# Kernel tuning notes

Measured on AMD Instinct MI355X. Metric: run time of the kernel, lower is better.

The kernel has to match this reference:

```python
import jax, jax.numpy as jnp
import numpy as np

N = 6144          # num utterances (graph nodes)
D = 128           # utt_embed_size
WIN = 10          # att_window_size
NUM_SPK = 8
N_EMO = 7


def _init(key, shape):
    fan_in = shape[0]
    return jax.random.normal(key, shape, dtype=jnp.float32) * (1.0 / np.sqrt(fan_in))


def setup_inputs() -> dict:
    key = jax.random.key(0)
    ks = jax.random.split(key, 20)
    inp = {
        "x": jax.random.normal(ks[0], (N, D), dtype=jnp.float32),
        "speakers": jax.random.randint(ks[1], (N,), 0, NUM_SPK, dtype=jnp.int32),
        # layer-1 relation GCN weights (pred / suc / same / diff)
        "W_pred1": _init(ks[2], (D, D)),
        "W_suc1": _init(ks[3], (D, D)),
        "W_same1": _init(ks[4], (D, D)),
        "W_diff1": _init(ks[5], (D, D)),
        # layer-2 relation GCN weights
        "W_pred2": _init(ks[6], (D, D)),
        "W_suc2": _init(ks[7], (D, D)),
        "W_same2": _init(ks[8], (D, D)),
        "W_diff2": _init(ks[9], (D, D)),
        "w_aggr_1": _init(ks[10], (D, D)),
        "w_aggr_2": _init(ks[11], (D, D)),
        "w_e1": _init(ks[12], (2 * D, D)),
        "b_e1": jnp.zeros((D,), dtype=jnp.float32),
        "w_e2": _init(ks[13], (D, N_EMO)),
        "b_e2": jnp.zeros((N_EMO,), dtype=jnp.float32),
        "w_s": _init(ks[14], (2 * D, N_EMO)),
        "b_s": jnp.zeros((N_EMO,), dtype=jnp.float32),
    }
    return inp


def reference(x, speakers, W_pred1, W_suc1, W_same1, W_diff1,
              W_pred2, W_suc2, W_same2, W_diff2,
              w_aggr_1, w_aggr_2, w_e1, b_e1, w_e2, b_e2, w_s, b_s):
    n = x.shape[0]
    idx = jnp.arange(n)
    # windowed dot-product attention; entries outside the window stay 0.0
    # BEFORE the softmax (faithful to the torch code: zeros, not -inf)
    band = jnp.abs(idx[:, None] - idx[None, :]) <= WIN
    scores = jnp.where(band, x @ x.T, 0.0)            # [N, N]
    attn = jax.nn.softmax(scores, axis=1)
    # relation masks
    same = (speakers[:, None] == speakers[None, :]).astype(x.dtype)
    pred = (idx[None, :] >= idx[:, None]).astype(x.dtype)   # triu incl diag
    suc = 1.0 - pred                                          # strict lower tri
    adjs = (same * pred * attn,        # same-speaker, predecessor
            same * suc * attn,         # same-speaker, successor
            (1.0 - same) * pred * attn,  # diff-speaker, predecessor
            (1.0 - same) * suc * attn)   # diff-speaker, successor

    def gcn(h, Ws):  # sum_k adj_k @ (h @ W_k)
        return sum(a @ (h @ w) for a, w in zip(adjs, Ws))

    d = jnp.diagonal(attn)[:, None]   # self-attention scale
    h1 = jax.nn.relu(gcn(x, (W_pred1, W_suc1, W_same1, W_diff1))
                     + (x @ w_aggr_1) * d)
    h2 = jax.nn.relu(gcn(h1, (W_pred2, W_suc2, W_same2, W_diff2))
                     + (h1 @ w_aggr_2) * d)
    h = jnp.concatenate([h2, x], axis=1)              # [N, 2D]
    emotion = jax.nn.relu(h @ w_e1 + b_e1) @ w_e2 + b_e2   # [N, 7]
    sentiment = h @ w_s + b_s                               # [N, 7]
    return emotion, sentiment
```

## Files before the change

kernel.cpp:

```cpp
#include <hip/hip_runtime.h>
#include <hip/hip_bf16.h>


#define NN   6144
#define DD   128
#define WINW 10
#define YST  168
#define TAB_OFF 27456
#define SS_OFF  33088
#define SM_BYTES 35904
#define NBLK 768
#define WS_W1T 0
#define WS_W2T 163840
#define WS_WE1 327680
#define WS_WE2 393216
#define WS_WST 397312
#define WS_H1  405504
#define WS_H2  1978368
#define BAR_OFF 3551232
#define F1_OFF 16384
#define F2_OFF 40960
#define BAR_BYTES 65536

typedef unsigned short u16;
typedef unsigned long long u64;
typedef __attribute__((ext_vector_type(8))) short bf16x8;
typedef __attribute__((ext_vector_type(4))) float f32x4;

__device__ __forceinline__ float b2f(u16 u) {
    return __uint_as_float(((unsigned int)u) << 16);
}
__device__ __forceinline__ u16 f2b(float f) {
    __hip_bfloat16 h = __float2bfloat16(f);
    return *reinterpret_cast<u16*>(&h);
}
__device__ __forceinline__ bf16x8 cvt8(const float* p) {
    float4 u = *reinterpret_cast<const float4*>(p);
    float4 v = *reinterpret_cast<const float4*>(p + 4);
    bf16x8 r;
    r[0] = (short)f2b(u.x); r[1] = (short)f2b(u.y);
    r[2] = (short)f2b(u.z); r[3] = (short)f2b(u.w);
    r[4] = (short)f2b(v.x); r[5] = (short)f2b(v.y);
    r[6] = (short)f2b(v.z); r[7] = (short)f2b(v.w);
    return r;
}
__device__ __forceinline__ void st_agent_u32(unsigned* p, unsigned v) {
    __hip_atomic_store(p, v, __ATOMIC_RELAXED, __HIP_MEMORY_SCOPE_AGENT);
}
__device__ __forceinline__ void st_agent_u64(u64* p, u64 v) {
    __hip_atomic_store(p, v, __ATOMIC_RELAXED, __HIP_MEMORY_SCOPE_AGENT);
}
__device__ __forceinline__ unsigned ld_agent_u32(const unsigned* p) {
    return __hip_atomic_load(p, __ATOMIC_RELAXED, __HIP_MEMORY_SCOPE_AGENT);
}
__device__ __forceinline__ unsigned add_agent_u32(unsigned* p, unsigned v) {
    return __hip_atomic_fetch_add(p, v, __ATOMIC_RELAXED,
                                  __HIP_MEMORY_SCOPE_AGENT);
}
__device__ __forceinline__ void poll_ge(unsigned* p, unsigned v) {
    while (ld_agent_u32(p) < v) __builtin_amdgcn_s_sleep(1);
}
__device__ __forceinline__ const float* sel5(int r,
    const float* a0, const float* a1, const float* a2,
    const float* a3, const float* a4) {
    return r == 0 ? a0 : r == 1 ? a1 : r == 2 ? a2 : r == 3 ? a3 : a4;
}

__device__ __forceinline__ void layer_tile(
    const float* __restrict__ x, const u16* __restrict__ Ab16,
    const u16* __restrict__ BT, const int* __restrict__ spk,
    u16* __restrict__ hout, int first_layer, int hb, int bm,
    char* smraw, int tid, char* gate, int bid)
{
    u16*   Ys  = (u16*)smraw;
    float* Xs  = (float*)smraw;
    int2*  tab = (int2*)(smraw + TAB_OFF);
    float* Ss  = (float*)(smraw + SS_OFF);
    const int wave = tid >> 6, lane = tid & 63;
    const int lm = lane & 15, quad = lane >> 4;
    const int wm = wave >> 1, wn = wave & 1;

    bf16x8 afr[2][4];

    if (first_layer) {
        #pragma unroll
        for (int it = 0; it < 7; ++it) {
            int f = tid + it * 256;
            if (f < 52 * 32) {
                int s = f >> 5, c = f & 31;
                int g = min(max(bm - WINW + s, 0), NN - 1);
                *reinterpret_cast<float4*>(&Xs[s * 132 + c * 4]) =
                    *reinterpret_cast<const float4*>(&x[(size_t)g * DD + c * 4]);
            }
        }
        __syncthreads();

        if (tid < 128) {
            const int il = tid >> 2, q = tid & 3;
            const float* xr = &Xs[(il + WINW) * 132 + q * 32];
            float4 xq[8];
            #pragma unroll
            for (int c = 0; c < 8; ++c)
                xq[c] = *reinterpret_cast<const float4*>(xr + c * 4);
            float po[21];
            #pragma unroll
            for (int o = 0; o < 21; ++o) {
                const float* jr = &Xs[(il + o) * 132 + q * 32];
                float a0 = 0.f, a1 = 0.f, a2 = 0.f, a3 = 0.f;
                #pragma unroll
                for (int c = 0; c < 8; ++c) {
                    float4 b = *reinterpret_cast<const float4*>(jr + c * 4);
                    a0 = fmaf(xq[c].x, b.x, a0); a1 = fmaf(xq[c].y, b.y, a1);
                    a2 = fmaf(xq[c].z, b.z, a2); a3 = fmaf(xq[c].w, b.w, a3);
                }
                po[o] = (a0 + a1) + (a2 + a3);
            }
            #pragma unroll
            for (int o = 0; o < 21; ++o) {
                po[o] += __shfl_xor(po[o], 1);
                po[o] += __shfl_xor(po[o], 2);
            }
            if (q == 0) {
                #pragma unroll
                for (int o = 0; o < 21; ++o) {
                    int jg = bm + il - WINW + o;
                    Ss[il * 22 + o] =
                        (jg >= 0 && jg < NN) ? po[o] : -1e30f;
                }
            }
        }
        __syncthreads();

        if (tid < 32) {
            int il = tid, i = bm + il;
            float m = 0.f;
            #pragma unroll
            for (int o = 0; o < 21; ++o) {
                float s = Ss[il * 22 + o];
                if (s > -1e29f) m = fmaxf(m, s);
            }
            int lo = i - WINW; if (lo < 0) lo = 0;
            int hi = i + WINW; if (hi > NN - 1) hi = NN - 1;
            float Z = (float)(NN - (hi - lo + 1)) * __expf(-m);
            float ev[21];
            #pragma unroll
            for (int o = 0; o < 21; ++o) {
                float s = Ss[il * 22 + o];
                ev[o] = (s > -1e29f) ? __expf(s - m) : 0.f;
                Z += ev[o];
            }
            float rz = 1.f / Z;
            #pragma unroll
            for (int o = 0; o < 21; ++o) Ss[il * 22 + o] = ev[o] * rz;
        }
        __syncthreads();

        #pragma unroll
        for (int rr = 0; rr < 3; ++rr) {
            int p = tid + rr * 256;
            if (p < 704) {
                int il = p / 22, e = p - il * 22;
                int i  = bm + il;
                int si = spk[i];
                float w; int off;
                if (e < 21) {
                    int j = i - WINW + e;
                    bool valid = (j >= 0) && (j < NN);
                    int jc  = valid ? j : i;
                    int sel = (spk[jc] == si) ? ((j >= i) ? 0 : 1)
                                              : ((j >= i) ? 2 : 3);
                    w   = valid ? Ss[il * 22 + e] : 0.f;
                    off = valid ? (il + e) * YST + sel * 32 : 0;
                } else {
                    w   = Ss[il * 22 + WINW];
                    off = (il + WINW) * YST + 4 * 32;
                }
                tab[p] = make_int2(__float_as_int(w), off);
            }
        }

        #pragma unroll
        for (int mt = 0; mt < 2; ++mt) {
            int rl = min((wm * 2 + mt) * 16 + lm, 51);
            #pragma unroll
            for (int s = 0; s < 4; ++s)
                afr[mt][s] = cvt8(&Xs[rl * 132 + s * 32 + quad * 8]);
        }
        __syncthreads();

        if (gate) {
            if (tid == 0) {
                unsigned g = (unsigned)bid >> 5;
                unsigned* gflag = (unsigned*)(gate + 8192 + g * 128);
                unsigned* rflag = (unsigned*)(gate + 12288);
                if ((bid & 31) == 0) {
                    poll_ge(rflag, 1u);
                    st_agent_u32(gflag, 1u);
                } else {
                    poll_ge(gflag, 1u);
                }
            }
            __syncthreads();
            __builtin_amdgcn_sched_barrier(0);
        }
    } else {
        #pragma unroll
        for (int mt = 0; mt < 2; ++mt) {
            int gr = min(max(bm - WINW + (wm * 2 + mt) * 16 + lm, 0), NN - 1);
            #pragma unroll
            for (int s = 0; s < 4; ++s)
                afr[mt][s] = *reinterpret_cast<const bf16x8*>(
                    Ab16 + (size_t)gr * DD + s * 32 + quad * 8);
        }
    }

    f32x4 acc[2][5];
    #pragma unroll
    for (int mt = 0; mt < 2; ++mt)
        #pragma unroll
        for (int n = 0; n < 5; ++n) acc[mt][n] = {0.f, 0.f, 0.f, 0.f};

    #pragma unroll
    for (int np = 0; np < 5; ++np) {
        int nt = wn * 5 + np;
        int gn = (nt >> 1) * 128 + hb * 32 + (nt & 1) * 16 + lm;
        #pragma unroll
        for (int s = 0; s < 4; ++s) {
            bf16x8 b = *reinterpret_cast<const bf16x8*>(
                BT + (size_t)gn * DD + s * 32 + quad * 8);
            acc[0][np] = __builtin_amdgcn_mfma_f32_16x16x32_bf16(afr[0][s], b, acc[0][np], 0, 0, 0);
            acc[1][np] = __builtin_amdgcn_mfma_f32_16x16x32_bf16(afr[1][s], b, acc[1][np], 0, 0, 0);
        }
    }
    #pragma unroll
    for (int mt = 0; mt < 2; ++mt)
        #pragma unroll
        for (int np = 0; np < 5; ++np) {
            int nt = wn * 5 + np;
            #pragma unroll
            for (int r = 0; r < 4; ++r) {
                int lr = (wm * 2 + mt) * 16 + quad * 4 + r;
                if (lr < 52) Ys[lr * YST + nt * 16 + lm] = f2b(acc[mt][np][r]);
            }
        }
    __syncthreads();

    {
        const int c0 = (tid & 7) * 4;
        const int il = tid >> 3;
        float a0 = 0.f, a1 = 0.f, a2 = 0.f, a3 = 0.f;
        const int2* tp = &tab[il * 22];
        #pragma unroll
        for (int e = 0; e < 22; ++e) {
            int2 t = tp[e];
            float w = __int_as_float(t.x);
            u64 y4 = *reinterpret_cast<const u64*>(Ys + t.y + c0);
            a0 = fmaf(w, b2f((u16)(y4 & 0xffff)), a0);
            a1 = fmaf(w, b2f((u16)((y4 >> 16) & 0xffff)), a1);
            a2 = fmaf(w, b2f((u16)((y4 >> 32) & 0xffff)), a2);
            a3 = fmaf(w, b2f((u16)(y4 >> 48)), a3);
        }
        int i = bm + il;
        u64 pk = (u64)f2b(fmaxf(a0, 0.f)) |
                 ((u64)f2b(fmaxf(a1, 0.f)) << 16) |
                 ((u64)f2b(fmaxf(a2, 0.f)) << 32) |
                 ((u64)f2b(fmaxf(a3, 0.f)) << 48);
        st_agent_u64(reinterpret_cast<u64*>(
            &hout[(size_t)i * DD + hb * 32 + c0]), pk);
    }
}

__global__ __launch_bounds__(256, 4) void fused_kernel(
    const float* __restrict__ x, const int* __restrict__ spk,
    const float* __restrict__ p0, const float* __restrict__ p1,
    const float* __restrict__ p2, const float* __restrict__ p3,
    const float* __restrict__ p4,
    const float* __restrict__ q0, const float* __restrict__ q1,
    const float* __restrict__ q2, const float* __restrict__ q3,
    const float* __restrict__ q4,
    const float* __restrict__ we1, const float* __restrict__ be1,
    const float* __restrict__ we2, const float* __restrict__ be2,
    const float* __restrict__ wss, const float* __restrict__ bss,
    float* __restrict__ out, char* __restrict__ ws)
{
    u16*   W1T   = (u16*)(ws + WS_W1T);
    u16*   W2T   = (u16*)(ws + WS_W2T);
    u16*   We1T  = (u16*)(ws + WS_WE1);
    u16*   we2T  = (u16*)(ws + WS_WE2);
    u16*   wsT   = (u16*)(ws + WS_WST);
    u16*   h1b   = (u16*)(ws + WS_H1);
    u16*   h2b   = (u16*)(ws + WS_H2);
    char*  bar   = ws + BAR_OFF;
    unsigned* flag1 = (unsigned*)(bar + F1_OFF);
    unsigned* flag2 = (unsigned*)(bar + F2_OFF);

    __shared__ __align__(16) char smraw[SM_BYTES];
    const int bid = blockIdx.x;
    const int tid = threadIdx.x;

    if (bid < 160) {
        unsigned* W1T32 = (unsigned*)W1T;
        unsigned* W2T32 = (unsigned*)W2T;
        int idx = bid * 256 + tid;
        int c = idx & 127, rk = idx >> 7;
        int r = rk >> 6, k2 = rk & 63, k = k2 * 2;
        const float* s1 = sel5(r, p0, p1, p2, p3, p4);
        const float* s2 = sel5(r, q0, q1, q2, q3, q4);
        unsigned v1 = (unsigned)f2b(s1[k * 128 + c]) |
                      ((unsigned)f2b(s1[(k + 1) * 128 + c]) << 16);
        unsigned v2 = (unsigned)f2b(s2[k * 128 + c]) |
                      ((unsigned)f2b(s2[(k + 1) * 128 + c]) << 16);
        int U = (r * 128 + c) * 64 + k2;
        st_agent_u32(&W1T32[U], v1);
        st_agent_u32(&W2T32[U], v2);
    } else if (bid < 192) {
        unsigned* We1T32 = (unsigned*)We1T;
        #pragma unroll
        for (int it = 0; it < 2; ++it) {
            int idx = (bid - 160) * 256 + tid + it * 8192;
            int n = idx & 127, k2 = idx >> 7, k = k2 * 2;
            unsigned v = (unsigned)f2b(we1[k * 128 + n]) |
                         ((unsigned)f2b(we1[(k + 1) * 128 + n]) << 16);
            st_agent_u32(&We1T32[n * 128 + k2], v);
        }
    } else if (bid == 192) {
        unsigned* we2T32 = (unsigned*)we2T;
        #pragma unroll
        for (int it = 0; it < 4; ++it) {
            int U = tid + it * 256;
            int n = U >> 6, kh = U & 63, k = kh * 2;
            float lo = n < 7 ? we2[k * 7 + n] : 0.f;
            float hi = n < 7 ? we2[(k + 1) * 7 + n] : 0.f;
            st_agent_u32(&we2T32[U],
                         (unsigned)f2b(lo) | ((unsigned)f2b(hi) << 16));
        }
    } else if (bid == 193) {
        unsigned* wsT32 = (unsigned*)wsT;
        #pragma unroll
        for (int it = 0; it < 8; ++it) {
            int U = tid + it * 256;
            int n = U >> 7, kh = U & 127, k = kh * 2;
            float lo = n < 7 ? wss[k * 7 + n] : 0.f;
            float hi = n < 7 ? wss[(k + 1) * 7 + n] : 0.f;
            st_agent_u32(&wsT32[U],
                         (unsigned)f2b(lo) | ((unsigned)f2b(hi) << 16));
        }
    }

    __syncthreads();
    if (tid == 0) {
        unsigned g = (unsigned)bid >> 5;
        unsigned* gctr = (unsigned*)(bar + g * 128);
        unsigned* rctr = (unsigned*)(bar + 4096);
        unsigned* rflag = (unsigned*)(bar + 12288);
        unsigned r = add_agent_u32(gctr, 1u);
        if (r == 31u) {
            unsigned rr = add_agent_u32(rctr, 1u);
            if (rr == 23u) st_agent_u32(rflag, 1u);
        }
    }

    const int hb = bid / 192, bmi = bid - hb * 192;
    const int bm = bmi * 32;
    layer_tile(x, nullptr, W1T, spk, h1b, 1, hb, bm, smraw, tid, bar, bid);

    __syncthreads();
    if (tid == 0) add_agent_u32(&flag1[bmi * 32], 1u);
    if (tid == 0) {
        if (bmi > 0)   poll_ge(&flag1[(bmi - 1) * 32], 4u);
        poll_ge(&flag1[bmi * 32], 4u);
        if (bmi < 191) poll_ge(&flag1[(bmi + 1) * 32], 4u);
    }
    __syncthreads();
    __builtin_amdgcn_sched_barrier(0);

    layer_tile(nullptr, h1b, W2T, spk, h2b, 0, hb, bm, smraw, tid, nullptr, bid);

    __syncthreads();
    if (tid == 0) add_agent_u32(&flag2[bmi * 32], 1u);

    if (bid < 384) {
        const int rt = (bid & ~15) | ((bid & 7) << 1) | ((bid >> 3) & 1);
        const int bmh = rt * 16;
        const int wave = tid >> 6, lane = tid & 63;
        const int lm = lane & 15, quad = lane >> 4;
        const int row = bmh + lm;

        bf16x8 afr[8];
        #pragma unroll
        for (int s = 4; s < 8; ++s)
            afr[s] = cvt8(&x[(size_t)row * DD + (s - 4) * 32 + quad * 8]);
        if (tid == 0) poll_ge(&flag2[(rt >> 1) * 32], 4u);
        __syncthreads();
        __builtin_amdgcn_sched_barrier(0);

        #pragma unroll
        for (int s = 0; s < 4; ++s)
            afr[s] = *reinterpret_cast<const bf16x8*>(
                &h2b[(size_t)row * DD + s * 32 + quad * 8]);

        float* Es = (float*)smraw;
        f32x4 accE[2], accS = {0.f, 0.f, 0.f, 0.f};
        #pragma unroll
        for (int n = 0; n < 2; ++n) accE[n] = {0.f, 0.f, 0.f, 0.f};

        #pragma unroll
        for (int s = 0; s < 8; ++s) {
            #pragma unroll
            for (int n = 0; n < 2; ++n) {
                int nt = wave * 2 + n;
                bf16x8 b = *reinterpret_cast<const bf16x8*>(
                    &We1T[(size_t)(nt * 16 + lm) * 256 + s * 32 + quad * 8]);
                accE[n] = __builtin_amdgcn_mfma_f32_16x16x32_bf16(afr[s], b, accE[n], 0, 0, 0);
            }
            if (wave == 0) {
                bf16x8 bsf = *reinterpret_cast<const bf16x8*>(
                    &wsT[(size_t)lm * 256 + s * 32 + quad * 8]);
                accS = __builtin_amdgcn_mfma_f32_16x16x32_bf16(afr[s], bsf, accS, 0, 0, 0);
            }
        }

        if (wave == 0 && lm < 7) {
            #pragma unroll
            for (int r = 0; r < 4; ++r) {
                int i = bmh + quad * 4 + r;
                out[(size_t)NN * 7 + (size_t)i * 7 + lm] = accS[r] + bss[lm];
            }
        }
        #pragma unroll
        for (int n = 0; n < 2; ++n) {
            int col = (wave * 2 + n) * 16 + lm;
            float bias = be1[col];
            #pragma unroll
            for (int r = 0; r < 4; ++r)
                Es[(quad * 4 + r) * 132 + col] = fmaxf(accE[n][r] + bias, 0.f);
        }
        __syncthreads();

        if (wave == 0) {
            f32x4 accM = {0.f, 0.f, 0.f, 0.f};
            #pragma unroll
            for (int s = 0; s < 4; ++s) {
                bf16x8 a = cvt8(&Es[lm * 132 + s * 32 + quad * 8]);
                bf16x8 b = *reinterpret_cast<const bf16x8*>(
                    &we2T[(size_t)lm * 128 + s * 32 + quad * 8]);
                accM = __builtin_amdgcn_mfma_f32_16x16x32_bf16(a, b, accM, 0, 0, 0);
            }
            if (lm < 7) {
                #pragma unroll
                for (int r = 0; r < 4; ++r) {
                    int i = bmh + quad * 4 + r;
                    out[(size_t)i * 7 + lm] = accM[r] + be2[lm];
                }
            }
        }
    }
}

extern "C" void kernel_launch(void* const* d_in, const int* in_sizes, int n_in,
                              void* d_out, int out_size, void* d_ws, size_t ws_size,
                              hipStream_t stream)
{
    const float* x   = (const float*)d_in[0];
    const int*   spk = (const int*)d_in[1];
    const float* Wp1 = (const float*)d_in[2];
    const float* Wu1 = (const float*)d_in[3];
    const float* Wm1 = (const float*)d_in[4];
    const float* Wd1 = (const float*)d_in[5];
    const float* Wp2 = (const float*)d_in[6];
    const float* Wu2 = (const float*)d_in[7];
    const float* Wm2 = (const float*)d_in[8];
    const float* Wd2 = (const float*)d_in[9];
    const float* wa1 = (const float*)d_in[10];
    const float* wa2 = (const float*)d_in[11];
    const float* we1 = (const float*)d_in[12];
    const float* be1 = (const float*)d_in[13];
    const float* we2 = (const float*)d_in[14];
    const float* be2 = (const float*)d_in[15];
    const float* wss = (const float*)d_in[16];
    const float* bss = (const float*)d_in[17];
    float* out = (float*)d_out;
    char*  ws  = (char*)d_ws;

    hipMemsetAsync(ws + BAR_OFF, 0, BAR_BYTES, stream);

    fused_kernel<<<dim3(NBLK), dim3(256), 0, stream>>>(
        x, spk, Wp1, Wu1, Wm1, Wd1, wa1, Wp2, Wu2, Wm2, Wd2, wa2,
        we1, be1, we2, be2, wss, bss, out, ws);
}
```

Measured before the change: 146.4 us.

## Recompute halo rows per block to remove inter-block layer barriers

Each block now owns 8 output rows and recomputes attention, layer-1 activations over a 28-row halo, and layer 2 entirely in LDS. This removes the global h1/h2 buffers and the cross-block flag polling between layers. Adjacency tables are regrouped by relation so each 128-column weight slice is applied in turn. The cost is redundant halo computation (about 3.5x the layer-1 rows) and lower occupancy from launch bounds 4 to 3 with more LDS.

```diff
diff --git a/kernel.cpp b/kernel.cpp
--- a/kernel.cpp
+++ b/kernel.cpp
@@ -5,22 +5,31 @@
 #define NN   6144
 #define DD   128
 #define WINW 10
-#define YST  168
-#define TAB_OFF 27456
-#define SS_OFF  33088
-#define SM_BYTES 35904
+#define OROWS 8
+#define SROWS 48
+#define HROWS 28
+#define XST  132
+#define YST2 132
+#define H1ST 136
 #define NBLK 768
+#define NPACK 194
+#define LDS_A    0
+#define LDS_SS   25344
+#define LDS_TAB1 27808
+#define LDS_ST1  32736
+#define LDS_TAB2 33408
+#define LDS_ST2  34816
+#define LDS_H1   35008
+#define LDS_H2   42624
+#define LDS_SPK  44800
+#define SM_BYTES 44992
 #define WS_W1T 0
 #define WS_W2T 163840
 #define WS_WE1 327680
 #define WS_WE2 393216
 #define WS_WST 397312
-#define WS_H1  405504
-#define WS_H2  1978368
 #define BAR_OFF 3551232
-#define F1_OFF 16384
-#define F2_OFF 40960
-#define BAR_BYTES 65536
+#define BAR_BYTES 16384
 
 typedef unsigned short u16;
 typedef unsigned long long u64;
@@ -47,9 +56,6 @@
 __device__ __forceinline__ void st_agent_u32(unsigned* p, unsigned v) {
     __hip_atomic_store(p, v, __ATOMIC_RELAXED, __HIP_MEMORY_SCOPE_AGENT);
 }
-__device__ __forceinline__ void st_agent_u64(u64* p, u64 v) {
-    __hip_atomic_store(p, v, __ATOMIC_RELAXED, __HIP_MEMORY_SCOPE_AGENT);
-}
 __device__ __forceinline__ unsigned ld_agent_u32(const unsigned* p) {
     return __hip_atomic_load(p, __ATOMIC_RELAXED, __HIP_MEMORY_SCOPE_AGENT);
 }
@@ -65,212 +71,18 @@
     const float* a3, const float* a4) {
     return r == 0 ? a0 : r == 1 ? a1 : r == 2 ? a2 : r == 3 ? a3 : a4;
 }
-
-__device__ __forceinline__ void layer_tile(
-    const float* __restrict__ x, const u16* __restrict__ Ab16,
-    const u16* __restrict__ BT, const int* __restrict__ spk,
-    u16* __restrict__ hout, int first_layer, int hb, int bm,
-    char* smraw, int tid, char* gate, int bid)
-{
-    u16*   Ys  = (u16*)smraw;
-    float* Xs  = (float*)smraw;
-    int2*  tab = (int2*)(smraw + TAB_OFF);
-    float* Ss  = (float*)(smraw + SS_OFF);
-    const int wave = tid >> 6, lane = tid & 63;
-    const int lm = lane & 15, quad = lane >> 4;
-    const int wm = wave >> 1, wn = wave & 1;
-
-    bf16x8 afr[2][4];
-
-    if (first_layer) {
-        #pragma unroll
-        for (int it = 0; it < 7; ++it) {
-            int f = tid + it * 256;
-            if (f < 52 * 32) {
-                int s = f >> 5, c = f & 31;
-                int g = min(max(bm - WINW + s, 0), NN - 1);
-                *reinterpret_cast<float4*>(&Xs[s * 132 + c * 4]) =
-                    *reinterpret_cast<const float4*>(&x[(size_t)g * DD + c * 4]);
-            }
-        }
-        __syncthreads();
-
-        if (tid < 128) {
-            const int il = tid >> 2, q = tid & 3;
-            const float* xr = &Xs[(il + WINW) * 132 + q * 32];
-            float4 xq[8];
-            #pragma unroll
-            for (int c = 0; c < 8; ++c)
-                xq[c] = *reinterpret_cast<const float4*>(xr + c * 4);
-            float po[21];
-            #pragma unroll
-            for (int o = 0; o < 21; ++o) {
-                const float* jr = &Xs[(il + o) * 132 + q * 32];
-                float a0 = 0.f, a1 = 0.f, a2 = 0.f, a3 = 0.f;
-                #pragma unroll
-                for (int c = 0; c < 8; ++c) {
-                    float4 b = *reinterpret_cast<const float4*>(jr + c * 4);
-                    a0 = fmaf(xq[c].x, b.x, a0); a1 = fmaf(xq[c].y, b.y, a1);
-                    a2 = fmaf(xq[c].z, b.z, a2); a3 = fmaf(xq[c].w, b.w, a3);
-                }
-                po[o] = (a0 + a1) + (a2 + a3);
-            }
-            #pragma unroll
-            for (int o = 0; o < 21; ++o) {
-                po[o] += __shfl_xor(po[o], 1);
-                po[o] += __shfl_xor(po[o], 2);
-            }
-            if (q == 0) {
-                #pragma unroll
-                for (int o = 0; o < 21; ++o) {
-                    int jg = bm + il - WINW + o;
-                    Ss[il * 22 + o] =
-                        (jg >= 0 && jg < NN) ? po[o] : -1e30f;
-                }
-            }
-        }
-        __syncthreads();
-
-        if (tid < 32) {
-            int il = tid, i = bm + il;
-            float m = 0.f;
-            #pragma unroll
-            for (int o = 0; o < 21; ++o) {
-                float s = Ss[il * 22 + o];
-                if (s > -1e29f) m = fmaxf(m, s);
-            }
-            int lo = i - WINW; if (lo < 0) lo = 0;
-            int hi = i + WINW; if (hi > NN - 1) hi = NN - 1;
-            float Z = (float)(NN - (hi - lo + 1)) * __expf(-m);
-            float ev[21];
-            #pragma unroll
-            for (int o = 0; o < 21; ++o) {
-                float s = Ss[il * 22 + o];
-                ev[o] = (s > -1e29f) ? __expf(s - m) : 0.f;
-                Z += ev[o];
-            }
-            float rz = 1.f / Z;
-            #pragma unroll
-            for (int o = 0; o < 21; ++o) Ss[il * 22 + o] = ev[o] * rz;
-        }
-        __syncthreads();
-
-        #pragma unroll
-        for (int rr = 0; rr < 3; ++rr) {
-            int p = tid + rr * 256;
-            if (p < 704) {
-                int il = p / 22, e = p - il * 22;
-                int i  = bm + il;
-                int si = spk[i];
-                float w; int off;
-                if (e < 21) {
-                    int j = i - WINW + e;
-                    bool valid = (j >= 0) && (j < NN);
-                    int jc  = valid ? j : i;
-                    int sel = (spk[jc] == si) ? ((j >= i) ? 0 : 1)
-                                              : ((j >= i) ? 2 : 3);
-                    w   = valid ? Ss[il * 22 + e] : 0.f;
-                    off = valid ? (il + e) * YST + sel * 32 : 0;
-                } else {
-                    w   = Ss[il * 22 + WINW];
-                    off = (il + WINW) * YST + 4 * 32;
-                }
-                tab[p] = make_int2(__float_as_int(w), off);
-            }
-        }
-
-        #pragma unroll
-        for (int mt = 0; mt < 2; ++mt) {
-            int rl = min((wm * 2 + mt) * 16 + lm, 51);
-            #pragma unroll
-            for (int s = 0; s < 4; ++s)
-                afr[mt][s] = cvt8(&Xs[rl * 132 + s * 32 + quad * 8]);
-        }
-        __syncthreads();
-
-        if (gate) {
-            if (tid == 0) {
-                unsigned g = (unsigned)bid >> 5;
-                unsigned* gflag = (unsigned*)(gate + 8192 + g * 128);
-                unsigned* rflag = (unsigned*)(gate + 12288);
-                if ((bid & 31) == 0) {
-                    poll_ge(rflag, 1u);
-                    st_agent_u32(gflag, 1u);
-                } else {
-                    poll_ge(gflag, 1u);
-                }
-            }
-            __syncthreads();
-            __builtin_amdgcn_sched_barrier(0);
-        }
-    } else {
-        #pragma unroll
-        for (int mt = 0; mt < 2; ++mt) {
-            int gr = min(max(bm - WINW + (wm * 2 + mt) * 16 + lm, 0), NN - 1);
-            #pragma unroll
-            for (int s = 0; s < 4; ++s)
-                afr[mt][s] = *reinterpret_cast<const bf16x8*>(
-                    Ab16 + (size_t)gr * DD + s * 32 + quad * 8);
-        }
-    }
-
-    f32x4 acc[2][5];
-    #pragma unroll
-    for (int mt = 0; mt < 2; ++mt)
-        #pragma unroll
-        for (int n = 0; n < 5; ++n) acc[mt][n] = {0.f, 0.f, 0.f, 0.f};
-
-    #pragma unroll
-    for (int np = 0; np < 5; ++np) {
-        int nt = wn * 5 + np;
-        int gn = (nt >> 1) * 128 + hb * 32 + (nt & 1) * 16 + lm;
-        #pragma unroll
-        for (int s = 0; s < 4; ++s) {
-            bf16x8 b = *reinterpret_cast<const bf16x8*>(
-                BT + (size_t)gn * DD + s * 32 + quad * 8);
-            acc[0][np] = __builtin_amdgcn_mfma_f32_16x16x32_bf16(afr[0][s], b, acc[0][np], 0, 0, 0);
-            acc[1][np] = __builtin_amdgcn_mfma_f32_16x16x32_bf16(afr[1][s], b, acc[1][np], 0, 0, 0);
-        }
-    }
-    #pragma unroll
-    for (int mt = 0; mt < 2; ++mt)
-        #pragma unroll
-        for (int np = 0; np < 5; ++np) {
-            int nt = wn * 5 + np;
-            #pragma unroll
-            for (int r = 0; r < 4; ++r) {
-                int lr = (wm * 2 + mt) * 16 + quad * 4 + r;
-                if (lr < 52) Ys[lr * YST + nt * 16 + lm] = f2b(acc[mt][np][r]);
-            }
-        }
-    __syncthreads();
-
-    {
-        const int c0 = (tid & 7) * 4;
-        const int il = tid >> 3;
-        float a0 = 0.f, a1 = 0.f, a2 = 0.f, a3 = 0.f;
-        const int2* tp = &tab[il * 22];
-        #pragma unroll
-        for (int e = 0; e < 22; ++e) {
-            int2 t = tp[e];
-            float w = __int_as_float(t.x);
-            u64 y4 = *reinterpret_cast<const u64*>(Ys + t.y + c0);
-            a0 = fmaf(w, b2f((u16)(y4 & 0xffff)), a0);
-            a1 = fmaf(w, b2f((u16)((y4 >> 16) & 0xffff)), a1);
-            a2 = fmaf(w, b2f((u16)((y4 >> 32) & 0xffff)), a2);
-            a3 = fmaf(w, b2f((u16)(y4 >> 48)), a3);
-        }
-        int i = bm + il;
-        u64 pk = (u64)f2b(fmaxf(a0, 0.f)) |
-                 ((u64)f2b(fmaxf(a1, 0.f)) << 16) |
-                 ((u64)f2b(fmaxf(a2, 0.f)) << 32) |
-                 ((u64)f2b(fmaxf(a3, 0.f)) << 48);
-        st_agent_u64(reinterpret_cast<u64*>(
-            &hout[(size_t)i * DD + hb * 32 + c0]), pk);
-    }
-}
-
-__global__ __launch_bounds__(256, 4) void fused_kernel(
+__device__ __forceinline__ void acc4_add(f32x4& a, float w, u64 y4) {
+    a[0] = fmaf(w, b2f((u16)(y4 & 0xffff)), a[0]);
+    a[1] = fmaf(w, b2f((u16)((y4 >> 16) & 0xffff)), a[1]);
+    a[2] = fmaf(w, b2f((u16)((y4 >> 32) & 0xffff)), a[2]);
+    a[3] = fmaf(w, b2f((u16)(y4 >> 48)), a[3]);
+}
+__device__ __forceinline__ u64 pack4_relu(f32x4 a) {
+    return (u64)f2b(fmaxf(a[0], 0.f)) | ((u64)f2b(fmaxf(a[1], 0.f)) << 16) |
+           ((u64)f2b(fmaxf(a[2], 0.f)) << 32) | ((u64)f2b(fmaxf(a[3], 0.f)) << 48);
+}
+
+__global__ __launch_bounds__(256, 3) void fused_kernel(
     const float* __restrict__ x, const int* __restrict__ spk,
     const float* __restrict__ p0, const float* __restrict__ p1,
     const float* __restrict__ p2, const float* __restrict__ p3,
@@ -283,20 +95,30 @@
     const float* __restrict__ wss, const float* __restrict__ bss,
     float* __restrict__ out, char* __restrict__ ws)
 {
-    u16*   W1T   = (u16*)(ws + WS_W1T);
-    u16*   W2T   = (u16*)(ws + WS_W2T);
-    u16*   We1T  = (u16*)(ws + WS_WE1);
-    u16*   we2T  = (u16*)(ws + WS_WE2);
-    u16*   wsT   = (u16*)(ws + WS_WST);
-    u16*   h1b   = (u16*)(ws + WS_H1);
-    u16*   h2b   = (u16*)(ws + WS_H2);
-    char*  bar   = ws + BAR_OFF;
-    unsigned* flag1 = (unsigned*)(bar + F1_OFF);
-    unsigned* flag2 = (unsigned*)(bar + F2_OFF);
+    u16* W1T  = (u16*)(ws + WS_W1T);
+    u16* W2T  = (u16*)(ws + WS_W2T);
+    u16* We1T = (u16*)(ws + WS_WE1);
+    u16* we2T = (u16*)(ws + WS_WE2);
+    u16* wsT  = (u16*)(ws + WS_WST);
+    char* bar = ws + BAR_OFF;
 
     __shared__ __align__(16) char smraw[SM_BYTES];
-    const int bid = blockIdx.x;
-    const int tid = threadIdx.x;
+    float* Xs  = (float*)(smraw + LDS_A);
+    u16*   Ys  = (u16*)(smraw + LDS_A);
+    float* Es  = (float*)(smraw + LDS_A);
+    float* Ss  = (float*)(smraw + LDS_SS);
+    int2*  tab1 = (int2*)(smraw + LDS_TAB1);
+    int*   st1  = (int*)(smraw + LDS_ST1);
+    int2*  tab2 = (int2*)(smraw + LDS_TAB2);
+    int*   st2  = (int*)(smraw + LDS_ST2);
+    u16*   h1   = (u16*)(smraw + LDS_H1);
+    u16*   h2   = (u16*)(smraw + LDS_H2);
+    int*   SpkS = (int*)(smraw + LDS_SPK);
+
+    const int bid = blockIdx.x, tid = threadIdx.x;
+    const int wave = tid >> 6, lane = tid & 63;
+    const int lm = lane & 15, quad = lane >> 4;
+    const int bm = bid * OROWS;
 
     if (bid < 160) {
         unsigned* W1T32 = (unsigned*)W1T;
@@ -346,60 +168,302 @@
                          (unsigned)f2b(lo) | ((unsigned)f2b(hi) << 16));
         }
     }
-
-    __syncthreads();
+    if (bid < NPACK) {
+        __syncthreads();
+        if (tid == 0) {
+            unsigned r = add_agent_u32((unsigned*)bar, 1u);
+            if (r == NPACK - 1) st_agent_u32((unsigned*)(bar + 4096), 1u);
+        }
+    }
+
+    #pragma unroll
+    for (int it = 0; it < 6; ++it) {
+        int f = tid + it * 256;
+        int s = f >> 5, c = f & 31;
+        int g = min(max(bm - 20 + s, 0), NN - 1);
+        *reinterpret_cast<float4*>(&Xs[s * XST + c * 4]) =
+            *reinterpret_cast<const float4*>(&x[(size_t)g * DD + c * 4]);
+    }
+    if (tid < SROWS) SpkS[tid] = spk[min(max(bm - 20 + tid, 0), NN - 1)];
+    __syncthreads();
+
+    if (tid < HROWS * 8) {
+        const int hs = tid >> 3, q = tid & 7;
+        const int gc = min(max(bm - 10 + hs, 0), NN - 1);
+        const float* xr = &Xs[(gc - bm + 20) * XST + q * 16];
+        float4 xq[4];
+        #pragma unroll
+        for (int c = 0; c < 4; ++c)
+            xq[c] = *reinterpret_cast<const float4*>(xr + c * 4);
+        float po[21];
+        #pragma unroll
+        for (int o = 0; o < 21; ++o) {
+            int jg = gc - 10 + o;
+            bool valid = (jg >= 0) && (jg < NN);
+            int jl = valid ? (jg - bm + 20) : (gc - bm + 20);
+            const float* jr = &Xs[jl * XST + q * 16];
+            float a0 = 0.f, a1 = 0.f, a2 = 0.f, a3 = 0.f;
+            #pragma unroll
+            for (int c = 0; c < 4; ++c) {
+                float4 b = *reinterpret_cast<const float4*>(jr + c * 4);
+                a0 = fmaf(xq[c].x, b.x, a0); a1 = fmaf(xq[c].y, b.y, a1);
+                a2 = fmaf(xq[c].z, b.z, a2); a3 = fmaf(xq[c].w, b.w, a3);
+            }
+            po[o] = (a0 + a1) + (a2 + a3);
+        }
+        #pragma unroll
+        for (int o = 0; o < 21; ++o) {
+            po[o] += __shfl_xor(po[o], 1);
+            po[o] += __shfl_xor(po[o], 2);
+            po[o] += __shfl_xor(po[o], 4);
+        }
+        if (q == 0) {
+            #pragma unroll
+            for (int o = 0; o < 21; ++o) {
+                int jg = gc - 10 + o;
+                Ss[hs * 22 + o] = (jg >= 0 && jg < NN) ? po[o] : -1e30f;
+            }
+        }
+    }
+    __syncthreads();
+
+    if (tid < HROWS) {
+        int hs = tid, i = min(max(bm - 10 + hs, 0), NN - 1);
+        float m = 0.f;
+        #pragma unroll
+        for (int o = 0; o < 21; ++o) {
+            float s = Ss[hs * 22 + o];
+            if (s > -1e29f) m = fmaxf(m, s);
+        }
+        int lo = i - WINW; if (lo < 0) lo = 0;
+        int hi = i + WINW; if (hi > NN - 1) hi = NN - 1;
+        float Z = (float)(NN - (hi - lo + 1)) * __expf(-m);
+        float ev[21];
+        #pragma unroll
+        for (int o = 0; o < 21; ++o) {
+            float s = Ss[hs * 22 + o];
+            ev[o] = (s > -1e29f) ? __expf(s - m) : 0.f;
+            Z += ev[o];
+        }
+        float rz = 1.f / Z;
+        #pragma unroll
+        for (int o = 0; o < 21; ++o) Ss[hs * 22 + o] = ev[o] * rz;
+    }
+    __syncthreads();
+
+    if (tid < HROWS) {
+        int hs = tid;
+        int gc = min(max(bm - 10 + hs, 0), NN - 1);
+        int si = SpkS[gc - bm + 20];
+        int idx = 0;
+        for (int p = 0; p < 5; ++p) {
+            st1[hs * 6 + p] = idx;
+            for (int e = 0; e < 22; ++e) {
+                int sel; float w; int off;
+                if (e < 21) {
+                    int j = gc - 10 + e;
+                    bool valid = (j >= 0) && (j < NN);
+                    int sj = valid ? SpkS[j - bm + 20] : si;
+                    sel = (sj == si) ? ((j >= gc) ? 0 : 1)
+                                     : ((j >= gc) ? 2 : 3);
+                    w   = valid ? Ss[hs * 22 + e] : 0.f;
+                    off = valid ? (j - bm + 20) * YST2 : 0;
+                } else {
+                    sel = 4; w = Ss[hs * 22 + 10];
+                    off = (gc - bm + 20) * YST2;
+                }
+                if (sel == p) {
+                    tab1[hs * 22 + idx] = make_int2(__float_as_int(w), off);
+                    ++idx;
+                }
+            }
+        }
+        st1[hs * 6 + 5] = idx;
+    } else if (tid >= 32 && tid < 32 + OROWS) {
+        int r = tid - 32;
+        int i = bm + r;
+        int si = SpkS[r + 30];
+        si = SpkS[r + 20];
+        int idx = 0;
+        for (int p = 0; p < 5; ++p) {
+            st2[r * 6 + p] = idx;
+            for (int e = 0; e < 22; ++e) {
+                int sel; float w; int off;
+                if (e < 21) {
+                    int j = i - 10 + e;
+                    bool valid = (j >= 0) && (j < NN);
+                    int sj = valid ? SpkS[j - bm + 20] : si;
+                    sel = (sj == si) ? ((j >= i) ? 0 : 1)
+                                     : ((j >= i) ? 2 : 3);
+                    w   = valid ? Ss[(r + 10) * 22 + e] : 0.f;
+                    off = valid ? (j - bm + 10) * YST2 : 0;
+                } else {
+                    sel = 4; w = Ss[(r + 10) * 22 + 10];
+                    off = (r + 10) * YST2;
+                }
+                if (sel == p) {
+                    tab2[r * 22 + idx] = make_int2(__float_as_int(w), off);
+                    ++idx;
+                }
+            }
+        }
+        st2[r * 6 + 5] = idx;
+    }
+
+    bf16x8 afr1[3][4];
+    #pragma unroll
+    for (int mt = 0; mt < 3; ++mt) {
+        int rl = mt * 16 + lm;
+        #pragma unroll
+        for (int ks = 0; ks < 4; ++ks)
+            afr1[mt][ks] = cvt8(&Xs[rl * XST + ks * 32 + quad * 8]);
+    }
+    __syncthreads();
+
     if (tid == 0) {
         unsigned g = (unsigned)bid >> 5;
-        unsigned* gctr = (unsigned*)(bar + g * 128);
-        unsigned* rctr = (unsigned*)(bar + 4096);
-        unsigned* rflag = (unsigned*)(bar + 12288);
-        unsigned r = add_agent_u32(gctr, 1u);
-        if (r == 31u) {
-            unsigned rr = add_agent_u32(rctr, 1u);
-            if (rr == 23u) st_agent_u32(rflag, 1u);
-        }
-    }
-
-    const int hb = bid / 192, bmi = bid - hb * 192;
-    const int bm = bmi * 32;
-    layer_tile(x, nullptr, W1T, spk, h1b, 1, hb, bm, smraw, tid, bar, bid);
-
-    __syncthreads();
-    if (tid == 0) add_agent_u32(&flag1[bmi * 32], 1u);
-    if (tid == 0) {
-        if (bmi > 0)   poll_ge(&flag1[(bmi - 1) * 32], 4u);
-        poll_ge(&flag1[bmi * 32], 4u);
-        if (bmi < 191) poll_ge(&flag1[(bmi + 1) * 32], 4u);
+        unsigned* gflag = (unsigned*)(bar + 8192 + g * 128);
+        unsigned* rflag = (unsigned*)(bar + 4096);
+        if ((bid & 31) == 0) {
+            poll_ge(rflag, 1u);
+            st_agent_u32(gflag, 1u);
+        } else {
+            poll_ge(gflag, 1u);
+        }
     }
     __syncthreads();
     __builtin_amdgcn_sched_barrier(0);
 
-    layer_tile(nullptr, h1b, W2T, spk, h2b, 0, hb, bm, smraw, tid, nullptr, bid);
-
-    __syncthreads();
-    if (tid == 0) add_agent_u32(&flag2[bmi * 32], 1u);
-
-    if (bid < 384) {
-        const int rt = (bid & ~15) | ((bid & 7) << 1) | ((bid >> 3) & 1);
-        const int bmh = rt * 16;
-        const int wave = tid >> 6, lane = tid & 63;
-        const int lm = lane & 15, quad = lane >> 4;
-        const int row = bmh + lm;
-
+    f32x4 hacc[4];
+    #pragma unroll
+    for (int k = 0; k < 4; ++k) hacc[k] = {0.f, 0.f, 0.f, 0.f};
+
+    for (int p = 0; p < 5; ++p) {
+        f32x4 accY[3][2];
+        #pragma unroll
+        for (int mt = 0; mt < 3; ++mt)
+            #pragma unroll
+            for (int j = 0; j < 2; ++j) accY[mt][j] = {0.f, 0.f, 0.f, 0.f};
+        #pragma unroll
+        for (int j = 0; j < 2; ++j) {
+            int gn = p * 128 + (wave * 2 + j) * 16 + lm;
+            #pragma unroll
+            for (int ks = 0; ks < 4; ++ks) {
+                bf16x8 b = *reinterpret_cast<const bf16x8*>(
+                    W1T + (size_t)gn * 128 + ks * 32 + quad * 8);
+                #pragma unroll
+                for (int mt = 0; mt < 3; ++mt)
+                    accY[mt][j] = __builtin_amdgcn_mfma_f32_16x16x32_bf16(
+                        afr1[mt][ks], b, accY[mt][j], 0, 0, 0);
+            }
+        }
+        #pragma unroll
+        for (int mt = 0; mt < 3; ++mt)
+            #pragma unroll
+            for (int j = 0; j < 2; ++j)
+                #pragma unroll
+                for (int r = 0; r < 4; ++r) {
+                    int lr = mt * 16 + quad * 4 + r;
+                    Ys[lr * YST2 + (wave * 2 + j) * 16 + lm] =
+                        f2b(accY[mt][j][r]);
+                }
+        __syncthreads();
+        #pragma unroll
+        for (int k = 0; k < 4; ++k) {
+            int slot = tid + k * 256;
+            if (slot < HROWS * 32) {
+                int hs = slot >> 5, c4 = slot & 31;
+                int s0 = st1[hs * 6 + p], s1 = st1[hs * 6 + p + 1];
+                for (int e = s0; e < s1; ++e) {
+                    int2 t = tab1[hs * 22 + e];
+                    u64 y4 = *reinterpret_cast<const u64*>(Ys + t.y + c4 * 4);
+                    acc4_add(hacc[k], __int_as_float(t.x), y4);
+                }
+            }
+        }
+        __syncthreads();
+    }
+    #pragma unroll
+    for (int k = 0; k < 4; ++k) {
+        int slot = tid + k * 256;
+        if (slot < HROWS * 32) {
+            int hs = slot >> 5, c4 = slot & 31;
+            *reinterpret_cast<u64*>(h1 + hs * H1ST + c4 * 4) =
+                pack4_relu(hacc[k]);
+        }
+    }
+    __syncthreads();
+
+    bf16x8 afr2[2][4];
+    #pragma unroll
+    for (int mt = 0; mt < 2; ++mt) {
+        int rl = min(mt * 16 + lm, HROWS - 1);
+        #pragma unroll
+        for (int ks = 0; ks < 4; ++ks)
+            afr2[mt][ks] = *reinterpret_cast<const bf16x8*>(
+                h1 + rl * H1ST + ks * 32 + quad * 8);
+    }
+
+    f32x4 h2acc = {0.f, 0.f, 0.f, 0.f};
+    for (int p = 0; p < 5; ++p) {
+        f32x4 accY[2][2];
+        #pragma unroll
+        for (int mt = 0; mt < 2; ++mt)
+            #pragma unroll
+            for (int j = 0; j < 2; ++j) accY[mt][j] = {0.f, 0.f, 0.f, 0.f};
+        #pragma unroll
+        for (int j = 0; j < 2; ++j) {
+            int gn = p * 128 + (wave * 2 + j) * 16 + lm;
+            #pragma unroll
+            for (int ks = 0; ks < 4; ++ks) {
+                bf16x8 b = *reinterpret_cast<const bf16x8*>(
+                    W2T + (size_t)gn * 128 + ks * 32 + quad * 8);
+                #pragma unroll
+                for (int mt = 0; mt < 2; ++mt)
+                    accY[mt][j] = __builtin_amdgcn_mfma_f32_16x16x32_bf16(
+                        afr2[mt][ks], b, accY[mt][j], 0, 0, 0);
+            }
+        }
+        #pragma unroll
+        for (int mt = 0; mt < 2; ++mt)
+            #pragma unroll
+            for (int j = 0; j < 2; ++j)
+                #pragma unroll
+                for (int r = 0; r < 4; ++r) {
+                    int lr = mt * 16 + quad * 4 + r;
+                    Ys[lr * YST2 + (wave * 2 + j) * 16 + lm] =
+                        f2b(accY[mt][j][r]);
+                }
+        __syncthreads();
+        {
+            int r2 = tid >> 5, c4 = tid & 31;
+            int s0 = st2[r2 * 6 + p], s1 = st2[r2 * 6 + p + 1];
+            for (int e = s0; e < s1; ++e) {
+                int2 t = tab2[r2 * 22 + e];
+                u64 y4 = *reinterpret_cast<const u64*>(Ys + t.y + c4 * 4);
+                acc4_add(h2acc, __int_as_float(t.x), y4);
+            }
+        }
+        __syncthreads();
+    }
+    {
+        int r2 = tid >> 5, c4 = tid & 31;
+        *reinterpret_cast<u64*>(h2 + r2 * H1ST + c4 * 4) = pack4_relu(h2acc);
+    }
+    __syncthreads();
+
+    {
         bf16x8 afr[8];
-        #pragma unroll
-        for (int s = 4; s < 8; ++s)
-            afr[s] = cvt8(&x[(size_t)row * DD + (s - 4) * 32 + quad * 8]);
-        if (tid == 0) poll_ge(&flag2[(rt >> 1) * 32], 4u);
-        __syncthreads();
-        __builtin_amdgcn_sched_barrier(0);
-
+        int hrow = min((int)lm, OROWS - 1);
         #pragma unroll
         for (int s = 0; s < 4; ++s)
             afr[s] = *reinterpret_cast<const bf16x8*>(
-                &h2b[(size_t)row * DD + s * 32 + quad * 8]);
-
-        float* Es = (float*)smraw;
+                h2 + hrow * H1ST + s * 32 + quad * 8);
+        int grx = min(bm + lm, NN - 1);
+        #pragma unroll
+        for (int s = 4; s < 8; ++s)
+            afr[s] = cvt8(&x[(size_t)grx * DD + (s - 4) * 32 + quad * 8]);
+
         f32x4 accE[2], accS = {0.f, 0.f, 0.f, 0.f};
         #pragma unroll
         for (int n = 0; n < 2; ++n) accE[n] = {0.f, 0.f, 0.f, 0.f};
@@ -420,10 +484,10 @@
             }
         }
 
-        if (wave == 0 && lm < 7) {
+        if (wave == 0 && lm < 7 && quad < 2) {
             #pragma unroll
             for (int r = 0; r < 4; ++r) {
-                int i = bmh + quad * 4 + r;
+                int i = bm + quad * 4 + r;
                 out[(size_t)NN * 7 + (size_t)i * 7 + lm] = accS[r] + bss[lm];
             }
         }
@@ -433,7 +497,7 @@
             float bias = be1[col];
             #pragma unroll
             for (int r = 0; r < 4; ++r)
-                Es[(quad * 4 + r) * 132 + col] = fmaxf(accE[n][r] + bias, 0.f);
+                Es[(quad * 4 + r) * XST + col] = fmaxf(accE[n][r] + bias, 0.f);
         }
         __syncthreads();
 
@@ -441,15 +505,15 @@
             f32x4 accM = {0.f, 0.f, 0.f, 0.f};
             #pragma unroll
             for (int s = 0; s < 4; ++s) {
-                bf16x8 a = cvt8(&Es[lm * 132 + s * 32 + quad * 8]);
+                bf16x8 a = cvt8(&Es[lm * XST + s * 32 + quad * 8]);
                 bf16x8 b = *reinterpret_cast<const bf16x8*>(
                     &we2T[(size_t)lm * 128 + s * 32 + quad * 8]);
                 accM = __builtin_amdgcn_mfma_f32_16x16x32_bf16(a, b, accM, 0, 0, 0);
             }
-            if (lm < 7) {
+            if (lm < 7 && quad < 2) {
                 #pragma unroll
                 for (int r = 0; r < 4; ++r) {
-                    int i = bmh + quad * 4 + r;
+                    int i = bm + quad * 4 + r;
                     out[(size_t)i * 7 + lm] = accM[r] + be2[lm];
                 }
             }
```

Result: slower. 159.5 us (+9.0%).
